# Performance work log

Hardware: AMD Instinct MI355X
Metric: run time of the kernel (lower is better)

## Reference

```python
import jax, jax.numpy as jnp
import numpy as np

DIM_IN = 256
HIDDEN = 32
NUM_EXPERTS = 64
N_TOKENS = 1048576
TEMP = 0.1
TOPK = 2


def setup_inputs() -> dict:
    key = jax.random.key(0)
    k_x, k_w1, k_b1, k_w2, k_b2 = jax.random.split(key, 5)
    s1 = 1.0 / np.sqrt(DIM_IN)
    s2 = 1.0 / np.sqrt(HIDDEN)
    return {
        "x": jax.random.normal(k_x, (N_TOKENS, DIM_IN), dtype=jnp.float32),
        "W1": jax.random.uniform(k_w1, (DIM_IN, HIDDEN), dtype=jnp.float32, minval=-s1, maxval=s1),
        "b1": jax.random.uniform(k_b1, (HIDDEN,), dtype=jnp.float32, minval=-s1, maxval=s1),
        "W2": jax.random.uniform(k_w2, (HIDDEN, NUM_EXPERTS), dtype=jnp.float32, minval=-s2, maxval=s2),
        "b2": jax.random.uniform(k_b2, (NUM_EXPERTS,), dtype=jnp.float32, minval=-s2, maxval=s2),
    }


def reference(x, W1, b1, W2, b2):
    # tiny 2-layer MLP router: [N, dim_in] -> [N, E]
    h = jnp.tanh(x @ W1 + b1)
    logits = h @ W2 + b2
    p_soft = jax.nn.softmax(logits / TEMP, axis=-1)

    # top-k mask + renormalize (no-grad branch in torch)
    p_ng = jax.lax.stop_gradient(p_soft)
    _, topk_idx = jax.lax.top_k(p_ng, TOPK)                 # [N, k]
    mask = jax.nn.one_hot(topk_idx, NUM_EXPERTS, dtype=p_soft.dtype).sum(axis=1)  # [N, E]
    p_hard = p_ng * mask
    p_hard = p_hard / (p_hard.sum(axis=-1, keepdims=True) + 1e-9)

    # straight-through combine: forward = p_hard, backward = p_soft
    w = p_soft + jax.lax.stop_gradient(p_hard - p_soft)
    return w
```

## Files before the change

kernel.cpp:

```cpp
#include <hip/hip_runtime.h>
#include <cfloat>

#define DIM_IN 256
#define HIDDEN 32
#define NE 64
#define ECH 16
#define BLOCK 256

__launch_bounds__(BLOCK, 4)
__global__ void router_fwd(const float* __restrict__ x,
                           const float* __restrict__ W1,
                           const float* __restrict__ b1,
                           const float* __restrict__ W2,
                           const float* __restrict__ b2,
                           float* __restrict__ out, int n) {
  __shared__ float obuf[BLOCK][ECH + 1];
  const int tid = threadIdx.x;
  const long t = (long)blockIdx.x * BLOCK + tid;
  const bool av = t < n;

  const float4* __restrict__ xr =
      reinterpret_cast<const float4*>(x + (av ? t : 0) * DIM_IN);

  float h[HIDDEN];
#pragma unroll
  for (int j = 0; j < HIDDEN; ++j) h[j] = 0.0f;

  float4 c0 = xr[0], c1 = xr[1], c2 = xr[2], c3 = xr[3];

#pragma unroll 1
  for (int g = 0; g < 16; ++g) {
    const int nb = (g < 15 ? g + 1 : 15) * 4;
    const float4 n0 = xr[nb + 0];
    const float4 n1 = xr[nb + 1];
    const float4 n2 = xr[nb + 2];
    const float4 n3 = xr[nb + 3];
    const float xs[16] = {c0.x, c0.y, c0.z, c0.w, c1.x, c1.y, c1.z, c1.w,
                          c2.x, c2.y, c2.z, c2.w, c3.x, c3.y, c3.z, c3.w};
    const float* __restrict__ wbase = W1 + g * 16 * HIDDEN;
#pragma unroll
    for (int k = 0; k < 16; ++k) {
      const float xv = xs[k];
      const float* __restrict__ wrow = wbase + k * HIDDEN;
#pragma unroll
      for (int j = 0; j < HIDDEN; ++j) h[j] = fmaf(xv, wrow[j], h[j]);
    }
    c0 = n0; c1 = n1; c2 = n2; c3 = n3;
  }

#pragma unroll
  for (int j = 0; j < HIDDEN; ++j) {
    const float v = h[j] + b1[j];
    const float e = __expf(2.0f * v);
    h[j] = 1.0f - 2.0f / (e + 1.0f);
  }

  float v1 = -FLT_MAX, v2 = -FLT_MAX, S = 0.0f;
  int i1 = 0, i2 = 0;

#pragma unroll 1
  for (int c = 0; c < NE / ECH; ++c) {
    float zc[ECH];
#pragma unroll
    for (int e = 0; e < ECH; ++e) zc[e] = 0.0f;
#pragma unroll
    for (int j = 0; j < HIDDEN; ++j) {
      const float hv = h[j];
      const float* __restrict__ wrow = W2 + j * NE + c * ECH;
#pragma unroll
      for (int e = 0; e < ECH; ++e) zc[e] = fmaf(hv, wrow[e], zc[e]);
    }
    const float m_prev = v1;
#pragma unroll
    for (int e = 0; e < ECH; ++e) {
      const float v = (zc[e] + b2[c * ECH + e]) * 10.0f;
      zc[e] = v;
      const int ge = c * ECH + e;
      const bool g1 = v > v1;
      const bool g2 = v > v2;
      v2 = g1 ? v1 : (g2 ? v : v2);
      i2 = g1 ? i1 : (g2 ? ge : i2);
      v1 = g1 ? v : v1;
      i1 = g1 ? ge : i1;
    }
    S *= __expf(m_prev - v1);
#pragma unroll
    for (int e = 0; e < ECH; ++e) S += __expf(zc[e] - v1);
  }

  const float pa = 1.0f / S;
  const float pb = __expf(v2 - v1) / S;
  const float d  = pa + pb + 1e-9f;
  const float oa = av ? pa / d : 0.0f;
  const float ob = av ? pb / d : 0.0f;

  const long obase = (long)blockIdx.x * BLOCK;
#pragma unroll 1
  for (int c = 0; c < NE / ECH; ++c) {
    __syncthreads();
#pragma unroll
    for (int e = 0; e < ECH; ++e) {
      const int ge = c * ECH + e;
      obuf[tid][e] = (ge == i1) ? oa : ((ge == i2) ? ob : 0.0f);
    }
    __syncthreads();
#pragma unroll
    for (int m = 0; m < 4; ++m) {
      const int f = m * BLOCK + tid;
      const int tok = f >> 2, part = f & 3;
      if (obase + tok < n) {
        float4 v;
        v.x = obuf[tok][part * 4 + 0];
        v.y = obuf[tok][part * 4 + 1];
        v.z = obuf[tok][part * 4 + 2];
        v.w = obuf[tok][part * 4 + 3];
        reinterpret_cast<float4*>(out + (obase + tok) * (long)NE + c * ECH)[part] = v;
      }
    }
  }
}

extern "C" void kernel_launch(void* const* d_in, const int* in_sizes, int n_in,
                              void* d_out, int out_size, void* d_ws, size_t ws_size,
                              hipStream_t stream) {
  const float* x  = (const float*)d_in[0];
  const float* W1 = (const float*)d_in[1];
  const float* b1 = (const float*)d_in[2];
  const float* W2 = (const float*)d_in[3];
  const float* b2 = (const float*)d_in[4];
  float* out = (float*)d_out;
  const int n_tokens = in_sizes[0] / DIM_IN;
  const int grid = (n_tokens + BLOCK - 1) / BLOCK;
  hipLaunchKernelGGL(router_fwd, dim3(grid), dim3(BLOCK), 0, stream,
                     x, W1, b1, W2, b2, out, n_tokens);
}
```

Before: 459.3 us.

## Replace LDS output transpose with wave shuffles, nontemporal x loads, higher occupancy

New measurement: 863.0 us. 1.88x slower.

```diff
diff --git a/kernel.cpp b/kernel.cpp
--- a/kernel.cpp
+++ b/kernel.cpp
@@ -4,39 +4,37 @@
 #define DIM_IN 256
 #define HIDDEN 32
 #define NE 64
-#define ECH 16
+#define ECH 8
 #define BLOCK 256
 
-__launch_bounds__(BLOCK, 4)
+typedef float f32x4 __attribute__((ext_vector_type(4)));
+
+__launch_bounds__(BLOCK, 8)
 __global__ void router_fwd(const float* __restrict__ x,
                            const float* __restrict__ W1,
                            const float* __restrict__ b1,
                            const float* __restrict__ W2,
                            const float* __restrict__ b2,
                            float* __restrict__ out, int n) {
-  __shared__ float obuf[BLOCK][ECH + 1];
   const int tid = threadIdx.x;
   const long t = (long)blockIdx.x * BLOCK + tid;
   const bool av = t < n;
 
-  const float4* __restrict__ xr =
-      reinterpret_cast<const float4*>(x + (av ? t : 0) * DIM_IN);
+  const f32x4* __restrict__ xr =
+      reinterpret_cast<const f32x4*>(x + (av ? t : 0) * (long)DIM_IN);
 
   float h[HIDDEN];
 #pragma unroll
   for (int j = 0; j < HIDDEN; ++j) h[j] = 0.0f;
 
-  float4 c0 = xr[0], c1 = xr[1], c2 = xr[2], c3 = xr[3];
-
 #pragma unroll 1
   for (int g = 0; g < 16; ++g) {
-    const int nb = (g < 15 ? g + 1 : 15) * 4;
-    const float4 n0 = xr[nb + 0];
-    const float4 n1 = xr[nb + 1];
-    const float4 n2 = xr[nb + 2];
-    const float4 n3 = xr[nb + 3];
-    const float xs[16] = {c0.x, c0.y, c0.z, c0.w, c1.x, c1.y, c1.z, c1.w,
-                          c2.x, c2.y, c2.z, c2.w, c3.x, c3.y, c3.z, c3.w};
+    const f32x4 q0 = __builtin_nontemporal_load(xr + g * 4 + 0);
+    const f32x4 q1 = __builtin_nontemporal_load(xr + g * 4 + 1);
+    const f32x4 q2 = __builtin_nontemporal_load(xr + g * 4 + 2);
+    const f32x4 q3 = __builtin_nontemporal_load(xr + g * 4 + 3);
+    const float xs[16] = {q0.x, q0.y, q0.z, q0.w, q1.x, q1.y, q1.z, q1.w,
+                          q2.x, q2.y, q2.z, q2.w, q3.x, q3.y, q3.z, q3.w};
     const float* __restrict__ wbase = W1 + g * 16 * HIDDEN;
 #pragma unroll
     for (int k = 0; k < 16; ++k) {
@@ -45,7 +43,6 @@
 #pragma unroll
       for (int j = 0; j < HIDDEN; ++j) h[j] = fmaf(xv, wrow[j], h[j]);
     }
-    c0 = n0; c1 = n1; c2 = n2; c3 = n3;
   }
 
 #pragma unroll
@@ -94,28 +91,26 @@
   const float oa = av ? pa / d : 0.0f;
   const float ob = av ? pb / d : 0.0f;
 
-  const long obase = (long)blockIdx.x * BLOCK;
+  const int lane = tid & 63;
+  const int wv   = tid >> 6;
+  const long wbase = (long)blockIdx.x * BLOCK + wv * 64;
+  const int e0 = (lane & 15) * 4;
 #pragma unroll 1
-  for (int c = 0; c < NE / ECH; ++c) {
-    __syncthreads();
-#pragma unroll
-    for (int e = 0; e < ECH; ++e) {
-      const int ge = c * ECH + e;
-      obuf[tid][e] = (ge == i1) ? oa : ((ge == i2) ? ob : 0.0f);
-    }
-    __syncthreads();
-#pragma unroll
-    for (int m = 0; m < 4; ++m) {
-      const int f = m * BLOCK + tid;
-      const int tok = f >> 2, part = f & 3;
-      if (obase + tok < n) {
-        float4 v;
-        v.x = obuf[tok][part * 4 + 0];
-        v.y = obuf[tok][part * 4 + 1];
-        v.z = obuf[tok][part * 4 + 2];
-        v.w = obuf[tok][part * 4 + 3];
-        reinterpret_cast<float4*>(out + (obase + tok) * (long)NE + c * ECH)[part] = v;
-      }
+  for (int m = 0; m < 16; ++m) {
+    const int src = m * 4 + (lane >> 4);
+    const float soa = __shfl(oa, src);
+    const float sob = __shfl(ob, src);
+    const int   si1 = __shfl(i1, src);
+    const int   si2 = __shfl(i2, src);
+    f32x4 v;
+    v.x = (e0 + 0 == si1) ? soa : ((e0 + 0 == si2) ? sob : 0.0f);
+    v.y = (e0 + 1 == si1) ? soa : ((e0 + 1 == si2) ? sob : 0.0f);
+    v.z = (e0 + 2 == si1) ? soa : ((e0 + 2 == si2) ? sob : 0.0f);
+    v.w = (e0 + 3 == si1) ? soa : ((e0 + 3 == si2) ? sob : 0.0f);
+    const long tok = wbase + m * 4 + (lane >> 4);
+    if (tok < n) {
+      f32x4* dst = reinterpret_cast<f32x4*>(out + (wbase + m * 4) * NE) + lane;
+      *dst = v;
     }
   }
 }
```
